# Kernel tuning notes

Measured on AMD Instinct MI355X. Metric: run time of the kernel, lower is better.

Reference implementation:

```python
import jax, jax.numpy as jnp
import numpy as np

N_DIMS = 4          # Euclidean GA with metric [1,1,1,1]
NUM_BLADES = 1 << N_DIMS  # 16 blades
B, N_IN, UNITS = 128, 512, 512


def _cayley_table(n_dims: int) -> np.ndarray:
    """Geometric-product Cayley table C[i,j,k] for Euclidean metric (+1,...,+1).

    Blades are indexed by bitmasks over the n basis vectors; e_A * e_B = sign * e_{A^B},
    where sign counts transpositions in the canonical reordering.
    """
    num = 1 << n_dims
    C = np.zeros((num, num, num), dtype=np.float32)
    for a in range(num):
        for b in range(num):
            t, swaps = a >> 1, 0
            while t:
                swaps += bin(t & b).count("1")
                t >>= 1
            C[a, b, a ^ b] = -1.0 if (swaps & 1) else 1.0
    return C


def setup_inputs() -> dict:
    key = jax.random.key(0)
    k1, k2, k3 = jax.random.split(key, 3)
    x = jax.random.normal(k1, (B, N_IN, NUM_BLADES), dtype=jnp.float32)
    w = jax.random.normal(k2, (UNITS, N_IN, NUM_BLADES), dtype=jnp.float32)
    b = jax.random.normal(k3, (UNITS, NUM_BLADES), dtype=jnp.float32)
    cayley = jnp.asarray(_cayley_table(N_DIMS))
    return {"x": x, "w": w, "b": b, "cayley": cayley}


def reference(x, w, b, cayley):
    # geom_prod(x[..., None, n, i], w[u, n, j])[..., u, n, k], summed over n, plus bias:
    # out[b,u,k] = sum_{n,i,j} x[b,n,i] * cayley[i,j,k] * w[u,n,j] + b[u,k]
    out = jnp.einsum("bni,ijk,unj->buk", x, cayley, w)
    return out + b
```

## Files before the change

### kernel.cpp

```cpp
#include <hip/hip_runtime.h>
#include <stdint.h>

typedef unsigned short ushort_t;
typedef __attribute__((ext_vector_type(8))) short short8v;
typedef __attribute__((ext_vector_type(4))) float f32x4;

#define AT_ELEMS (16u * 128u * 512u)
#define WT_ELEMS (16u * 512u * 512u)
#define WS_NEEDED ((size_t)(AT_ELEMS + WT_ELEMS) * 2u)

__host__ __device__ constexpr int ga_sign_i(int a, int b) {
  int t = a >> 1, sw = 0;
  while (t) {
    int x = t & b;
    while (x) { sw += x & 1; x >>= 1; }
    t >>= 1;
  }
  return (sw & 1) ? -1 : 1;
}

struct SignTab { int s[16][16]; };
constexpr SignTab make_tab() {
  SignTab t{};
  for (int i = 0; i < 16; i++)
    for (int j = 0; j < 16; j++) t.s[i][j] = ga_sign_i(i, j);
  return t;
}
constexpr SignTab STAB = make_tab();

__device__ __forceinline__ ushort_t f2bf(float f) {
  unsigned u = __float_as_uint(f);
  u = (u + 0x7FFFu + ((u >> 16) & 1u)) >> 16;
  return (ushort_t)u;
}

__device__ __forceinline__ short8v neg_bf16x8(short8v v) {
  const short m = (short)0x8000;
  return v ^ (short8v){m, m, m, m, m, m, m, m};
}

#define PREP_XT (128 * 512)
#define PREP_TOT (PREP_XT + 512 * 512)

__global__ __launch_bounds__(256) void prep_kernel(const float* __restrict__ x,
                                                   const float* __restrict__ w,
                                                   ushort_t* __restrict__ At,
                                                   ushort_t* __restrict__ Wt) {
  int tid = blockIdx.x * 256 + threadIdx.x;
  if (tid < PREP_XT) {
    int n = tid & 511, b = tid >> 9;
    const float4* xp = (const float4*)(x + (size_t)tid * 16);
    float v[16];
#pragma unroll
    for (int qq = 0; qq < 4; qq++) {
      float4 t = xp[qq];
      v[qq * 4 + 0] = t.x; v[qq * 4 + 1] = t.y; v[qq * 4 + 2] = t.z; v[qq * 4 + 3] = t.w;
    }
#pragma unroll
    for (int j = 0; j < 16; j++)
      At[((size_t)(j * 128 + b)) * 512 + n] = f2bf(v[j]);
  } else {
    int t = tid - PREP_XT;
    int n = t & 511, u = t >> 9;
    const float4* wp = (const float4*)(w + (size_t)t * 16);
    float v[16];
#pragma unroll
    for (int qq = 0; qq < 4; qq++) {
      float4 tt = wp[qq];
      v[qq * 4 + 0] = tt.x; v[qq * 4 + 1] = tt.y; v[qq * 4 + 2] = tt.z; v[qq * 4 + 3] = tt.w;
    }
#pragma unroll
    for (int j = 0; j < 16; j++)
      Wt[((size_t)(j * 512 + u)) * 512 + n] = f2bf(v[j]);
  }
}

__global__ __launch_bounds__(256, 1) void gemm_kernel(const ushort_t* __restrict__ At,
                                                      const ushort_t* __restrict__ Wt,
                                                      const float* __restrict__ bias,
                                                      float* __restrict__ out) {
  __shared__ __align__(16) ushort_t smem[65536];

  const int ut = blockIdx.x;
  const int bt = blockIdx.y;
  const int u0 = ut * 16, b0 = bt * 16;

  const int tid = threadIdx.x;
  const int wv = tid >> 6, lane = tid & 63;
  const int la = lane & 15, q = lane >> 4;

  const int srow = tid >> 4;
  const int sps = tid & 15;
  const int sp = sps ^ (srow & 7);
  const int sc = sp >> 2, sq = sp & 3;

  const ushort_t* AxB = At + (size_t)(b0 + srow) * 512 + sc * 32 + sq * 8;
  const ushort_t* WxB = Wt + (size_t)(u0 + srow) * 512 + sc * 32 + sq * 8;

  const int pr = wv * 4 + q;
  const int lbx = la * 256 + ((pr ^ (la & 7)) * 16);

  f32x4 acc[16];
#pragma unroll
  for (int k = 0; k < 16; k++) acc[k] = (f32x4){0.f, 0.f, 0.f, 0.f};

  const char* sm = (const char*)smem;

#pragma unroll 1
  for (int kt = 0; kt < 4; kt++) {
#pragma unroll
    for (int i = 0; i < 16; i++)
      __builtin_amdgcn_global_load_lds(
          (const __attribute__((address_space(1))) unsigned int*)(AxB + (size_t)i * 65536 + kt * 128),
          (__attribute__((address_space(3))) unsigned int*)(&smem[(i * 256 + wv * 64) * 8]),
          16, 0, 0);
#pragma unroll
    for (int i = 0; i < 16; i++)
      __builtin_amdgcn_global_load_lds(
          (const __attribute__((address_space(1))) unsigned int*)(WxB + (size_t)i * 262144 + kt * 128),
          (__attribute__((address_space(3))) unsigned int*)(&smem[32768 + (i * 256 + wv * 64) * 8]),
          16, 0, 0);
    __syncthreads();

    short8v av[16], nav[16];
#pragma unroll
    for (int i = 0; i < 16; i++) {
      av[i] = *(const short8v*)(sm + i * 4096 + lbx);
      nav[i] = neg_bf16x8(av[i]);
    }
#pragma unroll
    for (int j = 0; j < 16; j++) {
      const short8v bvj = *(const short8v*)(sm + 65536 + j * 4096 + lbx);
#pragma unroll
      for (int k = 0; k < 16; k++) {
        const int i = j ^ k;
        acc[k] = __builtin_amdgcn_mfma_f32_16x16x32_bf16(
            (STAB.s[i][j] < 0) ? nav[i] : av[i], bvj, acc[k], 0, 0, 0);
      }
    }
    __syncthreads();
  }

  float* red = (float*)smem;
#pragma unroll
  for (int g = 0; g < 4; g++) {
#pragma unroll
    for (int r2 = 0; r2 < 4; r2++) {
      float4 v = make_float4(acc[g * 4 + 0][r2], acc[g * 4 + 1][r2],
                             acc[g * 4 + 2][r2], acc[g * 4 + 3][r2]);
      int row = q * 4 + r2;
      *(float4*)&red[(((wv * 16 + row) * 16 + la) << 4) + g * 4] = v;
    }
  }
  __syncthreads();

  const int row = tid >> 4, col = tid & 15;
  float4 o[4];
#pragma unroll
  for (int g = 0; g < 4; g++)
    o[g] = *(const float4*)&bias[(u0 + col) * 16 + g * 4];
#pragma unroll
  for (int w2 = 0; w2 < 4; w2++) {
#pragma unroll
    for (int g = 0; g < 4; g++) {
      float4 v = *(const float4*)&red[(((w2 * 16 + row) * 16 + col) << 4) + g * 4];
      o[g].x += v.x; o[g].y += v.y; o[g].z += v.z; o[g].w += v.w;
    }
  }
#pragma unroll
  for (int g = 0; g < 4; g++)
    *(float4*)&out[((size_t)(b0 + row) * 512 + (u0 + col)) * 16 + g * 4] = o[g];
}

__global__ __launch_bounds__(256) void naive_kernel(const float* __restrict__ x,
                                                    const float* __restrict__ w,
                                                    const float* __restrict__ bias,
                                                    float* __restrict__ out) {
  int t = blockIdx.x * 256 + threadIdx.x;
  if (t >= 128 * 512 * 16) return;
  int k = t & 15;
  int u = (t >> 4) & 511;
  int b = t >> 13;
  float sgn[16];
#pragma unroll
  for (int i = 0; i < 16; i++) sgn[i] = (float)ga_sign_i(i, i ^ k);
  float acc = bias[u * 16 + k];
  for (int n = 0; n < 512; n++) {
    const float* xp = x + ((size_t)(b * 512 + n)) * 16;
    const float* wp = w + ((size_t)(u * 512 + n)) * 16;
#pragma unroll
    for (int i = 0; i < 16; i++)
      acc += xp[i] * sgn[i] * wp[i ^ k];
  }
  out[t] = acc;
}

extern "C" void kernel_launch(void* const* d_in, const int* in_sizes, int n_in,
                              void* d_out, int out_size, void* d_ws, size_t ws_size,
                              hipStream_t stream) {
  const float* x    = (const float*)d_in[0];
  const float* w    = (const float*)d_in[1];
  const float* bias = (const float*)d_in[2];
  float* out = (float*)d_out;

  if (ws_size >= WS_NEEDED && d_ws != nullptr) {
    ushort_t* At = (ushort_t*)d_ws;
    ushort_t* Wt = At + AT_ELEMS;

    prep_kernel<<<PREP_TOT / 256, 256, 0, stream>>>(x, w, At, Wt);
    gemm_kernel<<<dim3(32, 8), 256, 0, stream>>>(At, Wt, bias, out);
  } else {
    naive_kernel<<<(128 * 512 * 16) / 256, 256, 0, stream>>>(x, w, bias, out);
  }
}
```

Baseline: 94.54 us.

## Load GEMM operands directly from global memory into registers with A prefetch

The GEMM kernel stops staging A and W tiles through LDS with global_load_lds and barriers. Each lane now reads its MFMA fragments straight from global memory into registers, and A fragments are double-buffered so the next k-tile is prefetched while the current one is used. This removes LDS round-trips and per-iteration syncs, at the cost of much higher register pressure (about 48 short8 vectors live plus 16 accumulators) and less coalesced, uncached-in-LDS global reads. The loop is also fully unrolled.

```diff
diff --git a/kernel.cpp b/kernel.cpp
--- a/kernel.cpp
+++ b/kernel.cpp
@@ -79,7 +79,7 @@
                                                       const ushort_t* __restrict__ Wt,
                                                       const float* __restrict__ bias,
                                                       float* __restrict__ out) {
-  __shared__ __align__(16) ushort_t smem[65536];
+  __shared__ __align__(16) float red[16384];
 
   const int ut = blockIdx.x;
   const int bt = blockIdx.y;
@@ -89,59 +89,47 @@
   const int wv = tid >> 6, lane = tid & 63;
   const int la = lane & 15, q = lane >> 4;
 
-  const int srow = tid >> 4;
-  const int sps = tid & 15;
-  const int sp = sps ^ (srow & 7);
-  const int sc = sp >> 2, sq = sp & 3;
-
-  const ushort_t* AxB = At + (size_t)(b0 + srow) * 512 + sc * 32 + sq * 8;
-  const ushort_t* WxB = Wt + (size_t)(u0 + srow) * 512 + sc * 32 + sq * 8;
-
-  const int pr = wv * 4 + q;
-  const int lbx = la * 256 + ((pr ^ (la & 7)) * 16);
+  const ushort_t* Ax = At + (size_t)(b0 + la) * 512 + wv * 32 + q * 8;
+  const ushort_t* Wx = Wt + (size_t)(u0 + la) * 512 + wv * 32 + q * 8;
 
   f32x4 acc[16];
 #pragma unroll
   for (int k = 0; k < 16; k++) acc[k] = (f32x4){0.f, 0.f, 0.f, 0.f};
 
-  const char* sm = (const char*)smem;
-
-#pragma unroll 1
+  short8v av[2][16], bv[16], nav[16];
+
+#pragma unroll
+  for (int i = 0; i < 16; i++)
+    av[0][i] = *(const short8v*)(Ax + (size_t)i * 65536);
+
+#pragma unroll
   for (int kt = 0; kt < 4; kt++) {
-#pragma unroll
-    for (int i = 0; i < 16; i++)
-      __builtin_amdgcn_global_load_lds(
-          (const __attribute__((address_space(1))) unsigned int*)(AxB + (size_t)i * 65536 + kt * 128),
-          (__attribute__((address_space(3))) unsigned int*)(&smem[(i * 256 + wv * 64) * 8]),
-          16, 0, 0);
-#pragma unroll
-    for (int i = 0; i < 16; i++)
-      __builtin_amdgcn_global_load_lds(
-          (const __attribute__((address_space(1))) unsigned int*)(WxB + (size_t)i * 262144 + kt * 128),
-          (__attribute__((address_space(3))) unsigned int*)(&smem[32768 + (i * 256 + wv * 64) * 8]),
-          16, 0, 0);
-    __syncthreads();
-
-    short8v av[16], nav[16];
-#pragma unroll
-    for (int i = 0; i < 16; i++) {
-      av[i] = *(const short8v*)(sm + i * 4096 + lbx);
-      nav[i] = neg_bf16x8(av[i]);
-    }
+    const int cur = kt & 1, nxt = cur ^ 1;
+
+#pragma unroll
+    for (int j = 0; j < 16; j++)
+      bv[j] = *(const short8v*)(Wx + (size_t)j * 262144 + kt * 128);
+
+    if (kt < 3) {
+#pragma unroll
+      for (int i = 0; i < 16; i++)
+        av[nxt][i] = *(const short8v*)(Ax + (size_t)i * 65536 + (kt + 1) * 128);
+    }
+
+#pragma unroll
+    for (int i = 0; i < 16; i++) nav[i] = neg_bf16x8(av[cur][i]);
+
 #pragma unroll
     for (int j = 0; j < 16; j++) {
-      const short8v bvj = *(const short8v*)(sm + 65536 + j * 4096 + lbx);
 #pragma unroll
       for (int k = 0; k < 16; k++) {
         const int i = j ^ k;
         acc[k] = __builtin_amdgcn_mfma_f32_16x16x32_bf16(
-            (STAB.s[i][j] < 0) ? nav[i] : av[i], bvj, acc[k], 0, 0, 0);
+            (STAB.s[i][j] < 0) ? nav[i] : av[cur][i], bv[j], acc[k], 0, 0, 0);
       }
     }
-    __syncthreads();
-  }
-
-  float* red = (float*)smem;
+  }
+
 #pragma unroll
   for (int g = 0; g < 4; g++) {
 #pragma unroll
```

Result: slower. 108.6 us (+14.8%).

## Double-buffer LDS staging with smaller K chunks and split blades across waves

Applied to the files above, without the earlier changes.

The GEMM main loop now uses 8 smaller K stages with two LDS buffers, issuing the global-to-LDS loads for the next stage before computing on the current one, so memory latency overlaps the MFMA work. It also changes how work is split across waves: each wave handles half the K range of a chunk and half of the j blades, instead of a quarter of the K range and all 16 j blades. The idea is to hide load stalls that the earlier load-sync-compute-sync loop exposed. In exchange the loop uses the full 128KB LDS and relies on a manual vmcnt wait plus barrier for correctness. The same four-way cross-wave reduction is still used to combine the per-wave partial sums.

```diff
diff --git a/kernel.cpp b/kernel.cpp
--- a/kernel.cpp
+++ b/kernel.cpp
@@ -88,49 +88,57 @@
   const int tid = threadIdx.x;
   const int wv = tid >> 6, lane = tid & 63;
   const int la = lane & 15, q = lane >> 4;
-
-  const int srow = tid >> 4;
-  const int sps = tid & 15;
-  const int sp = sps ^ (srow & 7);
-  const int sc = sp >> 2, sq = sp & 3;
-
-  const ushort_t* AxB = At + (size_t)(b0 + srow) * 512 + sc * 32 + sq * 8;
-  const ushort_t* WxB = Wt + (size_t)(u0 + srow) * 512 + sc * 32 + sq * 8;
-
-  const int pr = wv * 4 + q;
-  const int lbx = la * 256 + ((pr ^ (la & 7)) * 16);
+  const int wn = wv >> 1, wj = wv & 1;
+
+  const int srow2 = tid >> 3;
+  const int ip = srow2 >> 4;
+  const int row = srow2 & 15;
+  const int sps = tid & 7;
+  const int sp = sps ^ (row & 7);
+
+  const ushort_t* Abase = At + (size_t)(ip * 128 + b0 + row) * 512 + sp * 8;
+  const ushort_t* Wbase = Wt + (size_t)(ip * 512 + u0 + row) * 512 + sp * 8;
+
+  const int lbx = la * 128 + ((((wn << 2) | q) ^ (la & 7)) * 16);
 
   f32x4 acc[16];
 #pragma unroll
   for (int k = 0; k < 16; k++) acc[k] = (f32x4){0.f, 0.f, 0.f, 0.f};
 
-  const char* sm = (const char*)smem;
+#define STAGE(BUFB, SN)                                                                       \
+  do {                                                                                        \
+    _Pragma("unroll")                                                                         \
+    for (int m = 0; m < 8; m++) {                                                             \
+      __builtin_amdgcn_global_load_lds(                                                       \
+          (const __attribute__((address_space(1))) unsigned int*)(Abase + (size_t)m * 131072 + (size_t)(SN) * 64), \
+          (__attribute__((address_space(3))) unsigned int*)(&smem[((BUFB) + m * 4096 + tid * 16) >> 1]),            \
+          16, 0, 0);                                                                          \
+      __builtin_amdgcn_global_load_lds(                                                       \
+          (const __attribute__((address_space(1))) unsigned int*)(Wbase + (size_t)m * 524288 + (size_t)(SN) * 64), \
+          (__attribute__((address_space(3))) unsigned int*)(&smem[((BUFB) + 32768 + m * 4096 + tid * 16) >> 1]),    \
+          16, 0, 0);                                                                          \
+    }                                                                                         \
+  } while (0)
+
+  STAGE(0, 0);
+  __syncthreads();
 
 #pragma unroll 1
-  for (int kt = 0; kt < 4; kt++) {
-#pragma unroll
-    for (int i = 0; i < 16; i++)
-      __builtin_amdgcn_global_load_lds(
-          (const __attribute__((address_space(1))) unsigned int*)(AxB + (size_t)i * 65536 + kt * 128),
-          (__attribute__((address_space(3))) unsigned int*)(&smem[(i * 256 + wv * 64) * 8]),
-          16, 0, 0);
-#pragma unroll
-    for (int i = 0; i < 16; i++)
-      __builtin_amdgcn_global_load_lds(
-          (const __attribute__((address_space(1))) unsigned int*)(WxB + (size_t)i * 262144 + kt * 128),
-          (__attribute__((address_space(3))) unsigned int*)(&smem[32768 + (i * 256 + wv * 64) * 8]),
-          16, 0, 0);
-    __syncthreads();
-
+  for (int s = 0; s < 8; s++) {
+    const int cb = (s & 1) << 16;
+    if (s < 7) STAGE(cb ^ 65536, s + 1);
+
+    const char* smb = (const char*)smem + cb;
     short8v av[16], nav[16];
 #pragma unroll
     for (int i = 0; i < 16; i++) {
-      av[i] = *(const short8v*)(sm + i * 4096 + lbx);
+      av[i] = *(const short8v*)(smb + i * 2048 + lbx);
       nav[i] = neg_bf16x8(av[i]);
     }
 #pragma unroll
-    for (int j = 0; j < 16; j++) {
-      const short8v bvj = *(const short8v*)(sm + 65536 + j * 4096 + lbx);
+    for (int jj = 0; jj < 8; jj++) {
+      const int j = wj * 8 + jj;
+      const short8v bvj = *(const short8v*)(smb + 32768 + j * 2048 + lbx);
 #pragma unroll
       for (int k = 0; k < 16; k++) {
         const int i = j ^ k;
@@ -138,8 +146,11 @@
             (STAB.s[i][j] < 0) ? nav[i] : av[i], bvj, acc[k], 0, 0, 0);
       }
     }
-    __syncthreads();
-  }
+
+    asm volatile("s_waitcnt vmcnt(0)" ::: "memory");
+    __builtin_amdgcn_s_barrier();
+  }
+#undef STAGE
 
   float* red = (float*)smem;
 #pragma unroll
@@ -148,13 +159,13 @@
     for (int r2 = 0; r2 < 4; r2++) {
       float4 v = make_float4(acc[g * 4 + 0][r2], acc[g * 4 + 1][r2],
                              acc[g * 4 + 2][r2], acc[g * 4 + 3][r2]);
-      int row = q * 4 + r2;
-      *(float4*)&red[(((wv * 16 + row) * 16 + la) << 4) + g * 4] = v;
+      int orow = q * 4 + r2;
+      *(float4*)&red[(((wv * 16 + orow) * 16 + la) << 4) + g * 4] = v;
     }
   }
   __syncthreads();
 
-  const int row = tid >> 4, col = tid & 15;
+  const int orow = tid >> 4, col = tid & 15;
   float4 o[4];
 #pragma unroll
   for (int g = 0; g < 4; g++)
@@ -163,13 +174,13 @@
   for (int w2 = 0; w2 < 4; w2++) {
 #pragma unroll
     for (int g = 0; g < 4; g++) {
-      float4 v = *(const float4*)&red[(((w2 * 16 + row) * 16 + col) << 4) + g * 4];
+      float4 v = *(const float4*)&red[(((w2 * 16 + orow) * 16 + col) << 4) + g * 4];
       o[g].x += v.x; o[g].y += v.y; o[g].z += v.z; o[g].w += v.w;
     }
   }
 #pragma unroll
   for (int g = 0; g < 4; g++)
-    *(float4*)&out[((size_t)(b0 + row) * 512 + (u0 + col)) * 16 + g * 4] = o[g];
+    *(float4*)&out[((size_t)(b0 + orow) * 512 + (u0 + col)) * 16 + g * 4] = o[g];
 }
 
 __global__ __launch_bounds__(256) void naive_kernel(const float* __restrict__ x,
```

Result: slower. 259.5 us (+174.5%).
